# Optimization experiments

Measured on AMD Instinct MI355X. Metric: run time of the kernel, lower is better.

## Reference

```python
import jax, jax.numpy as jnp
import numpy as np
from jax import lax

B, C, H, W = 4, 512, 32, 32
HEADS, HC, GROUPS = 8, 64, 4
GC = C // GROUPS          # group channels = 128
GH = HEADS // GROUPS      # heads per group = 2
KK = 5                    # offset conv kernel (stage_idx=2)
OFFSET_RANGE_FACTOR = 2.0
LN_EPS = 1e-5


def conv1x1(x, w, b):
    # x: [B,Cin,H,W], w: [Cout,Cin], b: [Cout]
    return jnp.einsum('bchw,oc->bohw', x, w) + b[None, :, None, None]


def ref_points(h, w, n, dtype=jnp.float32):
    # torch linspace(0.5, h-0.5, h) normalized to (-1,1); stacked (y,x)
    ry = ((jnp.arange(h, dtype=dtype) + 0.5) / h) * 2.0 - 1.0
    rx = ((jnp.arange(w, dtype=dtype) + 0.5) / w) * 2.0 - 1.0
    ref = jnp.stack(jnp.meshgrid(ry, rx, indexing='ij'), axis=-1)  # [h,w,2]
    return jnp.broadcast_to(ref[None], (n, h, w, 2))


def grid_sample(img, grid):
    # F.grid_sample: bilinear, align_corners=True, padding_mode='zeros'
    # img: [N,C,Hs,Ws], grid: [N,*S,2] with grid[...,0]=x, grid[...,1]=y in [-1,1]
    N, Cc, Hs, Ws = img.shape
    gx = (grid[..., 0] + 1.0) * 0.5 * (Ws - 1)
    gy = (grid[..., 1] + 1.0) * 0.5 * (Hs - 1)
    x0 = jnp.floor(gx)
    y0 = jnp.floor(gy)
    wx1 = gx - x0
    wy1 = gy - y0
    imgf = img.reshape(N, Cc, Hs * Ws)

    def corner(ix, iy, wgt):
        valid = ((ix >= 0) & (ix <= Ws - 1) & (iy >= 0) & (iy <= Hs - 1)).astype(img.dtype)
        flat = (jnp.clip(iy, 0, Hs - 1) * Ws + jnp.clip(ix, 0, Ws - 1)).astype(jnp.int32)
        vals = jax.vmap(lambda im, f: im[:, f])(imgf, flat)  # [N,C,*S]
        return vals * (wgt * valid)[:, None]

    return (corner(x0, y0, (1 - wx1) * (1 - wy1))
            + corner(x0 + 1, y0, wx1 * (1 - wy1))
            + corner(x0, y0 + 1, (1 - wx1) * wy1)
            + corner(x0 + 1, y0 + 1, wx1 * wy1))


def setup_inputs() -> dict:
    key = jax.random.key(0)
    ks = jax.random.split(key, 10)

    def w(k, shape, s=0.02):
        return jax.random.normal(k, shape, jnp.float32) * s

    return {
        'x': jax.random.normal(ks[0], (B, C, H, W), jnp.float32),
        'w_q': w(ks[1], (C, C)), 'b_q': jnp.zeros((C,), jnp.float32),
        'w_k': w(ks[2], (C, C)), 'b_k': jnp.zeros((C,), jnp.float32),
        'w_v': w(ks[3], (C, C)), 'b_v': jnp.zeros((C,), jnp.float32),
        'w_o': w(ks[4], (C, C)), 'b_o': jnp.zeros((C,), jnp.float32),
        'dw_w': w(ks[5], (GC, 1, KK, KK), 0.05),  # depthwise offset conv
        'dw_b': jnp.zeros((GC,), jnp.float32),
        'ln_g': jnp.ones((GC,), jnp.float32),
        'ln_b': jnp.zeros((GC,), jnp.float32),
        'off_w': w(ks[6], (2, GC), 0.05),          # 1x1 conv -> 2 offset channels
        'rpe': w(ks[7], (HEADS, 2 * H - 1, 2 * W - 1), 0.01),
    }


def reference(x, w_q, b_q, w_k, b_k, w_v, b_v, w_o, b_o,
              dw_w, dw_b, ln_g, ln_b, off_w, rpe):
    q = conv1x1(x, w_q, b_q)
    # 'b (g c) h w -> (b g) c h w'
    q_off = q.reshape(B * GROUPS, GC, H, W)
    # depthwise conv kk=5, stride=1, pad=2
    off = lax.conv_general_dilated(q_off, dw_w, (1, 1),
                                   ((KK // 2, KK // 2), (KK // 2, KK // 2)),
                                   dimension_numbers=('NCHW', 'OIHW', 'NCHW'),
                                   feature_group_count=GC) + dw_b[None, :, None, None]
    # LayerNormProxy over channel dim
    mu = jnp.mean(off, axis=1, keepdims=True)
    var = jnp.mean((off - mu) ** 2, axis=1, keepdims=True)
    off = (off - mu) * lax.rsqrt(var + LN_EPS) * ln_g[None, :, None, None] + ln_b[None, :, None, None]
    off = jax.nn.gelu(off, approximate=False)
    off = jnp.einsum('bchw,oc->bohw', off, off_w)  # [B*G, 2, Hk, Wk] (y,x channels)
    Hk, Wk = off.shape[2], off.shape[3]
    nS = Hk * Wk
    off_range = jnp.array([1.0 / Hk, 1.0 / Wk], dtype=x.dtype).reshape(1, 2, 1, 1)
    off = jnp.tanh(off) * off_range * OFFSET_RANGE_FACTOR
    off = jnp.transpose(off, (0, 2, 3, 1))  # [B*G, Hk, Wk, 2]
    ref = ref_points(Hk, Wk, B * GROUPS, x.dtype)
    pos = off + ref  # offset_range_factor >= 0 branch
    # deformable sampling (grid takes (x,y))
    xs = grid_sample(x.reshape(B * GROUPS, GC, H, W), pos[..., ::-1])  # [B*G,GC,Hk,Wk]
    xs = xs.reshape(B, C, 1, nS)
    qf = q.reshape(B * HEADS, HC, H * W)
    k = conv1x1(xs, w_k, b_k).reshape(B * HEADS, HC, nS)
    v = conv1x1(xs, w_v, b_v).reshape(B * HEADS, HC, nS)
    attn = jnp.einsum('bcm,bcn->bmn', qf, k) * (HC ** -0.5)  # [B*Hd, HW, nS]
    # continuous relative-position bias via bilinear table lookup
    rpe_b = jnp.broadcast_to(rpe[None], (B,) + rpe.shape).reshape(
        B * GROUPS, GH, rpe.shape[1], rpe.shape[2])
    q_grid = ref_points(H, W, B * GROUPS, x.dtype)
    disp = (q_grid.reshape(B * GROUPS, H * W, 1, 2)
            - pos.reshape(B * GROUPS, 1, nS, 2)) * 0.5  # [B*G, HW, nS, 2]
    bias = grid_sample(rpe_b, disp[..., ::-1]).reshape(B * HEADS, H * W, nS)
    attn = jax.nn.softmax(attn + bias, axis=2)
    out = jnp.einsum('bmn,bcn->bcm', attn, v).reshape(B, C, H, W)
    y = conv1x1(out, w_o, b_o)
    return (y,
            pos.reshape(B, GROUPS, Hk, Wk, 2),
            ref.reshape(B, GROUPS, Hk, Wk, 2))
```

## Files before the change

### kernel.cpp

```cpp
#include <hip/hip_runtime.h>
#include <hip/hip_bf16.h>

typedef __hip_bfloat16 bf16;
typedef __attribute__((ext_vector_type(8))) short bf16x8;
typedef __attribute__((ext_vector_type(4))) float f32x4;

#define BDIM 4
#define CDIM 512
#define NHEADS 8
#define NGROUPS 4
#define GCH 128

__device__ __forceinline__ float bf2f(bf16 v) { return __bfloat162float(v); }
__device__ __forceinline__ float bfu2f(unsigned short u) {
  return __uint_as_float(((unsigned)u) << 16);
}
__device__ __forceinline__ unsigned short f2bu(float v) {
  return __hip_bfloat16_raw(__float2bfloat16(v)).x;
}
__device__ __forceinline__ unsigned pack2(float lo, float hi) {
  return (unsigned)f2bu(lo) | ((unsigned)f2bu(hi) << 16);
}

template <bool IN_F32, typename OutT, int NMAT>
__global__ __launch_bounds__(256) void gemm_kernel(
    const float* __restrict__ W0, const float* __restrict__ bias0,
    const float* __restrict__ W1, const float* __restrict__ bias1,
    const void* __restrict__ in,
    OutT* __restrict__ out0, OutT* __restrict__ out1) {
  __shared__ __align__(16) unsigned char smem[8192 * (NMAT + 1)];
  unsigned char* b_lds = smem + 8192 * NMAT;
  const int b = blockIdx.z;
  const int o0 = blockIdx.y * 64;
  const int n0 = blockIdx.x * 64;
  const int t = threadIdx.x, l = t & 63, w = t >> 6;
  const int rg = l >> 4, cl = l & 15;
  const int o_base = (w >> 1) * 32, n_base = (w & 1) * 32;
  const int ao = t >> 2;
  const int ac8 = (t & 3) * 8;
  const int kc2 = (t & 31) * 2;
  const int kn8 = (t >> 5) * 8;
  const unsigned swo = (unsigned)((ao & 7) << 4);
  const float* Ws[2] = {W0, W1};
  const float* Bs[2] = {bias0, bias1};
  OutT* Os[2] = {out0, out1};

  f32x4 acc[NMAT][2][2];
#pragma unroll
  for (int m = 0; m < NMAT; m++)
#pragma unroll
    for (int i = 0; i < 2; i++)
#pragma unroll
      for (int j = 0; j < 2; j++) acc[m][i][j] = {0.f, 0.f, 0.f, 0.f};

  for (int k0 = 0; k0 < 512; k0 += 64) {
#pragma unroll
    for (int m = 0; m < NMAT; m++) {
      const float* wr = Ws[m] + (size_t)(o0 + ao) * 512 + k0;
      const float4 a0 = *(const float4*)(wr + ac8);
      const float4 a1 = *(const float4*)(wr + ac8 + 4);
      const float4 c0 = *(const float4*)(wr + ac8 + 32);
      const float4 c1 = *(const float4*)(wr + ac8 + 36);
      uint4 ua = {pack2(a0.x, a0.y), pack2(a0.z, a0.w),
                  pack2(a1.x, a1.y), pack2(a1.z, a1.w)};
      uint4 ub = {pack2(c0.x, c0.y), pack2(c0.z, c0.w),
                  pack2(c1.x, c1.y), pack2(c1.z, c1.w)};
      unsigned char* am = smem + 8192 * m;
      *(uint4*)(am + ao * 128 + ((2 * ac8) ^ swo)) = ua;
      *(uint4*)(am + ao * 128 + ((2 * ac8 + 64) ^ swo)) = ub;
    }
    if constexpr (IN_F32) {
      const float* inb = (const float*)in + (size_t)b * 524288;
      const float* p0 = inb + (size_t)(k0 + kc2) * 1024 + n0 + kn8;
      union { float4 v[2]; float f[8]; } r0, r1;
      r0.v[0] = *(const float4*)p0;
      r0.v[1] = *(const float4*)(p0 + 4);
      r1.v[0] = *(const float4*)(p0 + 1024);
      r1.v[1] = *(const float4*)(p0 + 1028);
#pragma unroll
      for (int i = 0; i < 8; i++) {
        const int n = kn8 + i;
        *(unsigned*)(b_lds + n * 128 + ((2 * kc2) ^ ((n & 7) << 4))) =
            pack2(r0.f[i], r1.f[i]);
      }
    } else {
      const unsigned short* inb = (const unsigned short*)in + (size_t)b * 524288;
      union { uint4 v; unsigned short hw[8]; } r0, r1;
      r0.v = *(const uint4*)(inb + (size_t)(k0 + kc2) * 1024 + n0 + kn8);
      r1.v = *(const uint4*)(inb + (size_t)(k0 + kc2 + 1) * 1024 + n0 + kn8);
#pragma unroll
      for (int i = 0; i < 8; i++) {
        const int n = kn8 + i;
        const unsigned v32 = (unsigned)r0.hw[i] | ((unsigned)r1.hw[i] << 16);
        *(unsigned*)(b_lds + n * 128 + ((2 * kc2) ^ ((n & 7) << 4))) = v32;
      }
    }
    __syncthreads();
#pragma unroll
    for (int kk = 0; kk < 2; kk++) {
      bf16x8 bfr[2];
#pragma unroll
      for (int nn = 0; nn < 2; nn++) {
        const int n_loc = n_base + 16 * nn + cl;
        bfr[nn] = *(const bf16x8*)(b_lds + n_loc * 128 +
                                   ((64 * kk + 16 * rg) ^ ((n_loc & 7) << 4)));
      }
#pragma unroll
      for (int m = 0; m < NMAT; m++) {
        bf16x8 af[2];
#pragma unroll
        for (int mi = 0; mi < 2; mi++) {
          const int o_loc = o_base + 16 * mi + cl;
          af[mi] = *(const bf16x8*)(smem + 8192 * m + o_loc * 128 +
                                    ((64 * kk + 16 * rg) ^ ((o_loc & 7) << 4)));
        }
#pragma unroll
        for (int mi = 0; mi < 2; mi++)
#pragma unroll
          for (int nn = 0; nn < 2; nn++)
            acc[m][mi][nn] = __builtin_amdgcn_mfma_f32_16x16x32_bf16(
                af[mi], bfr[nn], acc[m][mi][nn], 0, 0, 0);
      }
    }
    __syncthreads();
  }

  float* o_st = (float*)smem;
#pragma unroll
  for (int m = 0; m < NMAT; m++) {
    __syncthreads();
#pragma unroll
    for (int mi = 0; mi < 2; mi++)
#pragma unroll
      for (int nn = 0; nn < 2; nn++)
#pragma unroll
        for (int r = 0; r < 4; r++)
          o_st[(o_base + 16 * mi + 4 * rg + r) * 64 + n_base + 16 * nn + cl] =
              acc[m][mi][nn][r];
    __syncthreads();
    const int eo = t >> 4;
    const int en = (t & 15) * 4;
#pragma unroll
    for (int pass = 0; pass < 4; pass++) {
      const int o_loc = eo + pass * 16;
      const f32x4 v = *(const f32x4*)(o_st + o_loc * 64 + en);
      const float bv = Bs[m][o0 + o_loc];
      if constexpr (sizeof(OutT) == 2) {
        ushort4 u;
        u.x = f2bu(v[0] + bv);
        u.y = f2bu(v[1] + bv);
        u.z = f2bu(v[2] + bv);
        u.w = f2bu(v[3] + bv);
        *(ushort4*)((bf16*)Os[m] + ((size_t)b * 512 + o0 + o_loc) * 1024 + n0 + en) = u;
      } else {
        float4 r = {v[0] + bv, v[1] + bv, v[2] + bv, v[3] + bv};
        *(float4*)((float*)Os[m] + ((size_t)b * 512 + o0 + o_loc) * 1024 + n0 + en) = r;
      }
    }
  }
}

__global__ __launch_bounds__(1024) void offset_kernel(
    const bf16* __restrict__ q, const float* __restrict__ dw_w,
    const float* __restrict__ dw_b, const float* __restrict__ ln_g,
    const float* __restrict__ ln_b, const float* __restrict__ off_w,
    float* __restrict__ pos, float* __restrict__ out_pos, float* __restrict__ out_ref) {
  __shared__ unsigned short q_s[5][36][128];
  __shared__ float red_a[8][2][2];
  __shared__ float red_p[8][2][2];
  const int bg = blockIdx.x;
  const int h = blockIdx.y;
  const int b = bg >> 2, g = bg & 3;
  const int t = threadIdx.x;

  for (int task = t; task < 640; task += 1024) {
    const int ky = task >> 7, c = task & 127;
    const int y = h + ky - 2;
    if (y >= 0 && y < 32) {
      const unsigned short* qrow =
          (const unsigned short*)q + ((size_t)b * CDIM + g * GCH + c) * 1024 + y * 32;
      q_s[ky][0][c] = 0;
      q_s[ky][1][c] = 0;
#pragma unroll
      for (int x8 = 0; x8 < 4; x8++) {
        union { uint4 u; unsigned short s[8]; } vv;
        vv.u = *(const uint4*)(qrow + x8 * 8);
#pragma unroll
        for (int i = 0; i < 8; i++) q_s[ky][2 + x8 * 8 + i][c] = vv.s[i];
      }
      q_s[ky][34][c] = 0;
      q_s[ky][35][c] = 0;
    } else {
#pragma unroll
      for (int xi = 0; xi < 36; xi++) q_s[ky][xi][c] = 0;
    }
  }

  const int wslot = t >> 7;
  const int c = t & 127;
  const int half = c >> 6;
  const int lane = t & 63;
  float wgt[25];
#pragma unroll
  for (int i = 0; i < 25; i++) wgt[i] = dw_w[c * 25 + i];
  const float cbias = dw_b[c];
  const float gam = ln_g[c], bet = ln_b[c];
  const float ow0 = off_w[c], ow1 = off_w[GCH + c];
  __syncthreads();

  for (int j = 0; j < 4; j++) {
    const int w = wslot * 4 + j;
    float s = cbias;
#pragma unroll
    for (int ky = 0; ky < 5; ky++)
#pragma unroll
      for (int kx = 0; kx < 5; kx++)
        s += wgt[ky * 5 + kx] * bfu2f(q_s[ky][w + kx][c]);
    float ssum = s, ssq = s * s;
#pragma unroll
    for (int o = 1; o < 64; o <<= 1) {
      ssum += __shfl_xor(ssum, o);
      ssq += __shfl_xor(ssq, o);
    }
    if (lane == 0) { red_a[wslot][half][0] = ssum; red_a[wslot][half][1] = ssq; }
    __syncthreads();
    const float mu = (red_a[wslot][0][0] + red_a[wslot][1][0]) * (1.0f / 128.0f);
    const float var = (red_a[wslot][0][1] + red_a[wslot][1][1]) * (1.0f / 128.0f) - mu * mu;
    const float xn = (s - mu) * rsqrtf(var + 1e-5f) * gam + bet;
    const float ge = 0.5f * xn * (1.0f + erff(xn * 0.70710678118654752f));
    float p0 = ow0 * ge, p1 = ow1 * ge;
#pragma unroll
    for (int o = 1; o < 64; o <<= 1) {
      p0 += __shfl_xor(p0, o);
      p1 += __shfl_xor(p1, o);
    }
    if (lane == 0) { red_p[wslot][half][0] = p0; red_p[wslot][half][1] = p1; }
    __syncthreads();
    if (c == 0) {
      const float oy = tanhf(red_p[wslot][0][0] + red_p[wslot][1][0]) * 0.0625f;
      const float ox = tanhf(red_p[wslot][0][1] + red_p[wslot][1][1]) * 0.0625f;
      const float ry = ((float)h + 0.5f) * (2.0f / 32.0f) - 1.0f;
      const float rx = ((float)w + 0.5f) * (2.0f / 32.0f) - 1.0f;
      const float py = oy + ry, px = ox + rx;
      const size_t idx = (size_t)bg * 1024 + h * 32 + w;
      pos[idx * 2] = py;
      pos[idx * 2 + 1] = px;
      out_pos[idx * 2] = py;
      out_pos[idx * 2 + 1] = px;
      out_ref[idx * 2] = ry;
      out_ref[idx * 2 + 1] = rx;
    }
  }
}

__global__ __launch_bounds__(256) void sample_kernel(
    const float* __restrict__ x, const float* __restrict__ pos, bf16* __restrict__ xs) {
  const int bg = blockIdx.x, c = blockIdx.y;
  const int b = bg >> 2, g = bg & 3;
  __shared__ float plane[1024];
  const float* xp = x + ((size_t)b * CDIM + g * GCH + c) * 1024;
  for (int i = threadIdx.x; i < 1024; i += 256) plane[i] = xp[i];
  __syncthreads();
  for (int s = threadIdx.x; s < 1024; s += 256) {
    const float py = pos[((size_t)bg * 1024 + s) * 2];
    const float px = pos[((size_t)bg * 1024 + s) * 2 + 1];
    const float gx = (px + 1.0f) * 15.5f;
    const float gy = (py + 1.0f) * 15.5f;
    const float x0f = floorf(gx), y0f = floorf(gy);
    const float wx = gx - x0f, wy = gy - y0f;
    const int ix = (int)x0f, iy = (int)y0f;
    float r = 0.0f;
    const bool vx0 = (ix >= 0) & (ix <= 31), vx1 = (ix + 1 >= 0) & (ix + 1 <= 31);
    const bool vy0 = (iy >= 0) & (iy <= 31), vy1 = (iy + 1 >= 0) & (iy + 1 <= 31);
    if (vy0 && vx0) r += plane[iy * 32 + ix] * (1.0f - wx) * (1.0f - wy);
    if (vy0 && vx1) r += plane[iy * 32 + ix + 1] * wx * (1.0f - wy);
    if (vy1 && vx0) r += plane[(iy + 1) * 32 + ix] * (1.0f - wx) * wy;
    if (vy1 && vx1) r += plane[(iy + 1) * 32 + ix + 1] * wx * wy;
    xs[((size_t)bg * GCH + c) * 1024 + s] = __float2bfloat16(r);
  }
}

__global__ __launch_bounds__(512) void attn_kernel(
    const bf16* __restrict__ q, const bf16* __restrict__ kk,
    const bf16* __restrict__ vv, const float* __restrict__ pos,
    const float* __restrict__ rpe, bf16* __restrict__ ao) {
  __shared__ __align__(16) unsigned char smem[68360];
  float* rpe_f = (float*)(smem + 49152);
  float* m_x = (float*)(smem + 67336);
  float* s_x = (float*)(smem + 67848);

  const int bh = blockIdx.y;
  const int m0 = blockIdx.x * 64;
  const int b = bh >> 3, h = bh & 7;
  const int g = h >> 1;
  const int bg = b * 4 + g;
  const int t = threadIdx.x, l = t & 63, w = t >> 6;
  const int wq = w & 3, half = w >> 2;
  const int rg = l >> 4, cl = l & 15;
  const int t2 = t & 255;
  const size_t hbase = ((size_t)b * CDIM + h * 64) * 1024;
  const unsigned short* qu = (const unsigned short*)q;

  unsigned char* k_base = smem + half * 8192;
  unsigned char* v_base = smem + 16384 + half * 8192;
  unsigned char* p_base = smem + 32768 + half * 8192;
  float* pos_a = (float*)(smem + 66312) + half * 128;

  for (int i = t; i < 65 * 66; i += 512) {
    const int y = i / 66, x = i - y * 66;
    float v = 0.0f;
    if (y >= 1 && y <= 63 && x >= 1 && x <= 63)
      v = rpe[h * 3969 + (y - 1) * 63 + (x - 1)];
    rpe_f[i] = v;
  }

  const int qloc = 16 * wq + cl;
  const int qm = m0 + qloc;
  const float qy15 = 15.5f * (((float)(qm >> 5) + 0.5f) * (2.0f / 32.0f) - 1.0f);
  const float qx15 = 15.5f * (((float)(qm & 31) + 0.5f) * (2.0f / 32.0f) - 1.0f);

  bf16x8 bq[2];
#pragma unroll
  for (int kc = 0; kc < 2; kc++) {
    bf16x8 a;
#pragma unroll
    for (int j = 0; j < 8; j++)
      a[j] = (short)qu[hbase + (size_t)(32 * kc + 8 * rg + j) * 1024 + qm];
    bq[kc] = a;
  }

  float rmax = -1e30f, rsum = 0.0f;
  f32x4 oacc[4] = {{0.f,0.f,0.f,0.f},{0.f,0.f,0.f,0.f},
                   {0.f,0.f,0.f,0.f},{0.f,0.f,0.f,0.f}};

  const float* posb = pos + (size_t)bg * 2048;
  const unsigned swl = (unsigned)((cl & 7) << 4);
  const int kc2 = (t2 & 31) * 2;
  const int kn8 = (t2 >> 5) * 8;
  const int vc = t2 >> 2;
  const int vh = (t2 & 3) * 32;

  for (int tile = 0; tile < 8; tile++) {
    const int n0 = half * 512 + tile * 64;
    {
      union { uint4 v; unsigned short hw[8]; } r0, r1;
      r0.v = *(const uint4*)(kk + hbase + (size_t)kc2 * 1024 + n0 + kn8);
      r1.v = *(const uint4*)(kk + hbase + (size_t)(kc2 + 1) * 1024 + n0 + kn8);
#pragma unroll
      for (int i = 0; i < 8; i++) {
        const int n = kn8 + i;
        const unsigned v32 = (unsigned)r0.hw[i] | ((unsigned)r1.hw[i] << 16);
        *(unsigned*)(k_base + n * 128 + ((kc2 * 2) ^ ((n & 7) << 4))) = v32;
      }
      const uint4 s0 = *(const uint4*)(vv + hbase + (size_t)vc * 1024 + n0 + vh / 2);
      const uint4 s1 = *(const uint4*)(vv + hbase + (size_t)vc * 1024 + n0 + vh / 2 + 8);
      *(uint4*)(v_base + vc * 128 + (vh ^ ((vc & 7) << 4))) = s0;
      *(uint4*)(v_base + vc * 128 + ((vh + 16) ^ ((vc & 7) << 4))) = s1;
      if (t2 < 128) pos_a[t2] = 31.0f - 15.5f * posb[2 * n0 + t2];
    }
    __syncthreads();

    f32x4 sf[4];
#pragma unroll
    for (int tn = 0; tn < 4; tn++) {
      const int nrow = 16 * tn + cl;
      const bf16x8 a0 = *(const bf16x8*)(k_base + nrow * 128 + ((16 * rg) ^ swl));
      const bf16x8 a1 = *(const bf16x8*)(k_base + nrow * 128 + ((64 + 16 * rg) ^ swl));
      f32x4 z = {0.f, 0.f, 0.f, 0.f};
      z = __builtin_amdgcn_mfma_f32_16x16x32_bf16(a0, bq[0], z, 0, 0, 0);
      z = __builtin_amdgcn_mfma_f32_16x16x32_bf16(a1, bq[1], z, 0, 0, 0);
      sf[tn] = z;
    }

#pragma unroll
    for (int tn = 0; tn < 4; tn++)
#pragma unroll
      for (int r = 0; r < 4; r++) {
        const int key = 16 * tn + 4 * rg + r;
        const float gyc = qy15 + pos_a[2 * key];
        const float gxc = qx15 + pos_a[2 * key + 1];
        const float y0f = floorf(gyc), x0f = floorf(gxc);
        const float wy = gyc - y0f, wx = gxc - x0f;
        const int iy1 = (int)y0f + 1, ix1 = (int)x0f + 1;
        const float* tp = rpe_f + iy1 * 66 + ix1;
        const float t00 = tp[0], t01 = tp[1];
        const float t10 = tp[66], t11 = tp[67];
        const float r0v = t00 + (t01 - t00) * wx;
        const float r1v = t10 + (t11 - t10) * wx;
        const float bias = r0v + (r1v - r0v) * wy;
        sf[tn][r] = sf[tn][r] * 0.125f + bias;
      }

    float tmax = sf[0][0];
#pragma unroll
    for (int tn = 0; tn < 4; tn++)
#pragma unroll
      for (int r = 0; r < 4; r++) tmax = fmaxf(tmax, sf[tn][r]);
    tmax = fmaxf(tmax, __shfl_xor(tmax, 16));
    tmax = fmaxf(tmax, __shfl_xor(tmax, 32));
    const float nmax = fmaxf(rmax, tmax);
    const float corr = __expf(rmax - nmax);
    rmax = nmax;
    float lsum = 0.0f;
    unsigned pw[8];
#pragma unroll
    for (int tn = 0; tn < 4; tn++) {
      const float p0 = __expf(sf[tn][0] - nmax);
      const float p1 = __expf(sf[tn][1] - nmax);
      const float p2 = __expf(sf[tn][2] - nmax);
      const float p3 = __expf(sf[tn][3] - nmax);
      lsum += (p0 + p1) + (p2 + p3);
      pw[2 * tn] = pack2(p0, p1);
      pw[2 * tn + 1] = pack2(p2, p3);
    }
    lsum += __shfl_xor(lsum, 16);
    lsum += __shfl_xor(lsum, 32);
    rsum = rsum * corr + lsum;
#pragma unroll
    for (int tc = 0; tc < 4; tc++) {
      oacc[tc][0] *= corr; oacc[tc][1] *= corr;
      oacc[tc][2] *= corr; oacc[tc][3] *= corr;
    }

#pragma unroll
    for (int tn = 0; tn < 4; tn++) {
      *(unsigned*)(p_base + qloc * 128 + ((2 * (16 * tn + 4 * rg)) ^ swl)) = pw[2 * tn];
      *(unsigned*)(p_base + qloc * 128 + ((2 * (16 * tn + 4 * rg) + 4) ^ swl)) = pw[2 * tn + 1];
    }

#pragma unroll
    for (int kc = 0; kc < 2; kc++) {
      const bf16x8 pb = *(const bf16x8*)(p_base + qloc * 128 + ((2 * (32 * kc + 8 * rg)) ^ swl));
#pragma unroll
      for (int tc = 0; tc < 4; tc++) {
        const int crow = 16 * tc + cl;
        const bf16x8 av = *(const bf16x8*)(v_base + crow * 128 + ((2 * (32 * kc + 8 * rg)) ^ swl));
        oacc[tc] = __builtin_amdgcn_mfma_f32_16x16x32_bf16(av, pb, oacc[tc], 0, 0, 0);
      }
    }
    __syncthreads();
  }

  if (l < 16) {
    m_x[half * 64 + wq * 16 + cl] = rmax;
    s_x[half * 64 + wq * 16 + cl] = rsum;
  }
  __syncthreads();
  const float m0v = m_x[wq * 16 + cl], m1v = m_x[64 + wq * 16 + cl];
  const float s0v = s_x[wq * 16 + cl], s1v = s_x[64 + wq * 16 + cl];
  const float M = fmaxf(m0v, m1v);
  const float f0 = __expf(m0v - M), f1 = __expf(m1v - M);
  const float inv = 1.0f / (f0 * s0v + f1 * s1v);
  const float scale = (half == 0 ? f0 : f1) * inv;
  float* o_st = (float*)smem;
  if (half == 0) {
#pragma unroll
    for (int tc = 0; tc < 4; tc++)
#pragma unroll
      for (int r = 0; r < 4; r++)
        o_st[(16 * tc + 4 * rg + r) * 66 + qloc] = oacc[tc][r] * scale;
  }
  __syncthreads();
  if (half == 1) {
#pragma unroll
    for (int tc = 0; tc < 4; tc++)
#pragma unroll
      for (int r = 0; r < 4; r++)
        o_st[(16 * tc + 4 * rg + r) * 66 + qloc] += oacc[tc][r] * scale;
  }
  __syncthreads();
  {
    const int c = t >> 3, mq = (t & 7) * 8;
    unsigned u[4];
#pragma unroll
    for (int i = 0; i < 4; i++)
      u[i] = pack2(o_st[c * 66 + mq + 2 * i], o_st[c * 66 + mq + 2 * i + 1]);
    uint4 outv = {u[0], u[1], u[2], u[3]};
    *(uint4*)(ao + hbase + (size_t)c * 1024 + m0 + mq) = outv;
  }
}

extern "C" void kernel_launch(void* const* d_in, const int* in_sizes, int n_in,
                              void* d_out, int out_size, void* d_ws, size_t ws_size,
                              hipStream_t stream) {
  const float* x    = (const float*)d_in[0];
  const float* w_q  = (const float*)d_in[1];
  const float* b_q  = (const float*)d_in[2];
  const float* w_k  = (const float*)d_in[3];
  const float* b_k  = (const float*)d_in[4];
  const float* w_v  = (const float*)d_in[5];
  const float* b_v  = (const float*)d_in[6];
  const float* w_o  = (const float*)d_in[7];
  const float* b_o  = (const float*)d_in[8];
  const float* dw_w = (const float*)d_in[9];
  const float* dw_b = (const float*)d_in[10];
  const float* ln_g = (const float*)d_in[11];
  const float* ln_b = (const float*)d_in[12];
  const float* off_w= (const float*)d_in[13];
  const float* rpe  = (const float*)d_in[14];

  float* out_y   = (float*)d_out;
  float* out_pos = out_y + 2097152;
  float* out_ref = out_pos + 32768;

  float* pos_ws = (float*)d_ws;
  bf16*  q_ws   = (bf16*)(pos_ws + 32768);
  bf16*  xs_ws  = q_ws + 2097152;
  bf16*  k_ws   = xs_ws + 2097152;
  bf16*  v_ws   = k_ws + 2097152;
  bf16*  ao_ws  = xs_ws;

  gemm_kernel<true, bf16, 1><<<dim3(16, 8, 4), 256, 0, stream>>>(
      w_q, b_q, nullptr, nullptr, x, q_ws, (bf16*)nullptr);
  offset_kernel<<<dim3(16, 32), 1024, 0, stream>>>(q_ws, dw_w, dw_b, ln_g, ln_b, off_w,
                                                   pos_ws, out_pos, out_ref);
  sample_kernel<<<dim3(16, 128), 256, 0, stream>>>(x, pos_ws, xs_ws);
  gemm_kernel<false, bf16, 2><<<dim3(16, 8, 4), 256, 0, stream>>>(
      w_k, b_k, w_v, b_v, xs_ws, k_ws, v_ws);
  attn_kernel<<<dim3(16, 32), 512, 0, stream>>>(q_ws, k_ws, v_ws, pos_ws, rpe, ao_ws);
  gemm_kernel<false, float, 1><<<dim3(16, 8, 4), 256, 0, stream>>>(
      w_o, b_o, nullptr, nullptr, ao_ws, out_y, (float*)nullptr);
}
```

Measured before the change: 111.8 us.

## Split GEMM K dimension across two thread halves with LDS reduction

Measured after the change: 114.3 us. +2.3%, slower.

```diff
diff --git a/kernel.cpp b/kernel.cpp
--- a/kernel.cpp
+++ b/kernel.cpp
@@ -23,27 +23,30 @@
 }
 
 template <bool IN_F32, typename OutT, int NMAT>
-__global__ __launch_bounds__(256) void gemm_kernel(
+__global__ __launch_bounds__(512) void gemm_kernel(
     const float* __restrict__ W0, const float* __restrict__ bias0,
     const float* __restrict__ W1, const float* __restrict__ bias1,
     const void* __restrict__ in,
     OutT* __restrict__ out0, OutT* __restrict__ out1) {
-  __shared__ __align__(16) unsigned char smem[8192 * (NMAT + 1)];
-  unsigned char* b_lds = smem + 8192 * NMAT;
+  __shared__ __align__(16) unsigned char smem[16384 * (NMAT + 1)];
   const int b = blockIdx.z;
   const int o0 = blockIdx.y * 64;
   const int n0 = blockIdx.x * 64;
   const int t = threadIdx.x, l = t & 63, w = t >> 6;
+  const int ks = t >> 8;
+  const int t2 = t & 255;
+  const int quad = w & 3;
   const int rg = l >> 4, cl = l & 15;
-  const int o_base = (w >> 1) * 32, n_base = (w & 1) * 32;
-  const int ao = t >> 2;
-  const int ac8 = (t & 3) * 8;
-  const int kc2 = (t & 31) * 2;
-  const int kn8 = (t >> 5) * 8;
+  const int o_base = (quad >> 1) * 32, n_base = (quad & 1) * 32;
+  const int ao = t2 >> 2;
+  const int ac8 = (t2 & 3) * 8;
+  const int kc2 = (t2 & 31) * 2;
+  const int kn8 = (t2 >> 5) * 8;
   const unsigned swo = (unsigned)((ao & 7) << 4);
   const float* Ws[2] = {W0, W1};
   const float* Bs[2] = {bias0, bias1};
   OutT* Os[2] = {out0, out1};
+  unsigned char* bl = smem + NMAT * 16384 + ks * 8192;
 
   f32x4 acc[NMAT][2][2];
 #pragma unroll
@@ -53,7 +56,8 @@
 #pragma unroll
       for (int j = 0; j < 2; j++) acc[m][i][j] = {0.f, 0.f, 0.f, 0.f};
 
-  for (int k0 = 0; k0 < 512; k0 += 64) {
+  for (int it = 0; it < 4; it++) {
+    const int k0 = ks * 256 + it * 64;
 #pragma unroll
     for (int m = 0; m < NMAT; m++) {
       const float* wr = Ws[m] + (size_t)(o0 + ao) * 512 + k0;
@@ -65,7 +69,7 @@
                   pack2(a1.x, a1.y), pack2(a1.z, a1.w)};
       uint4 ub = {pack2(c0.x, c0.y), pack2(c0.z, c0.w),
                   pack2(c1.x, c1.y), pack2(c1.z, c1.w)};
-      unsigned char* am = smem + 8192 * m;
+      unsigned char* am = smem + (m * 2 + ks) * 8192;
       *(uint4*)(am + ao * 128 + ((2 * ac8) ^ swo)) = ua;
       *(uint4*)(am + ao * 128 + ((2 * ac8 + 64) ^ swo)) = ub;
     }
@@ -80,7 +84,7 @@
 #pragma unroll
       for (int i = 0; i < 8; i++) {
         const int n = kn8 + i;
-        *(unsigned*)(b_lds + n * 128 + ((2 * kc2) ^ ((n & 7) << 4))) =
+        *(unsigned*)(bl + n * 128 + ((2 * kc2) ^ ((n & 7) << 4))) =
             pack2(r0.f[i], r1.f[i]);
       }
     } else {
@@ -92,7 +96,7 @@
       for (int i = 0; i < 8; i++) {
         const int n = kn8 + i;
         const unsigned v32 = (unsigned)r0.hw[i] | ((unsigned)r1.hw[i] << 16);
-        *(unsigned*)(b_lds + n * 128 + ((2 * kc2) ^ ((n & 7) << 4))) = v32;
+        *(unsigned*)(bl + n * 128 + ((2 * kc2) ^ ((n & 7) << 4))) = v32;
       }
     }
     __syncthreads();
@@ -102,7 +106,7 @@
 #pragma unroll
       for (int nn = 0; nn < 2; nn++) {
         const int n_loc = n_base + 16 * nn + cl;
-        bfr[nn] = *(const bf16x8*)(b_lds + n_loc * 128 +
+        bfr[nn] = *(const bf16x8*)(bl + n_loc * 128 +
                                    ((64 * kk + 16 * rg) ^ ((n_loc & 7) << 4)));
       }
 #pragma unroll
@@ -111,7 +115,7 @@
 #pragma unroll
         for (int mi = 0; mi < 2; mi++) {
           const int o_loc = o_base + 16 * mi + cl;
-          af[mi] = *(const bf16x8*)(smem + 8192 * m + o_loc * 128 +
+          af[mi] = *(const bf16x8*)(smem + (m * 2 + ks) * 8192 + o_loc * 128 +
                                     ((64 * kk + 16 * rg) ^ ((o_loc & 7) << 4)));
         }
 #pragma unroll
@@ -128,33 +132,45 @@
   float* o_st = (float*)smem;
 #pragma unroll
   for (int m = 0; m < NMAT; m++) {
-    __syncthreads();
-#pragma unroll
-    for (int mi = 0; mi < 2; mi++)
-#pragma unroll
-      for (int nn = 0; nn < 2; nn++)
-#pragma unroll
-        for (int r = 0; r < 4; r++)
-          o_st[(o_base + 16 * mi + 4 * rg + r) * 64 + n_base + 16 * nn + cl] =
-              acc[m][mi][nn][r];
-    __syncthreads();
-    const int eo = t >> 4;
-    const int en = (t & 15) * 4;
-#pragma unroll
-    for (int pass = 0; pass < 4; pass++) {
-      const int o_loc = eo + pass * 16;
-      const f32x4 v = *(const f32x4*)(o_st + o_loc * 64 + en);
+    if (m) __syncthreads();
+    if (ks == 0) {
+#pragma unroll
+      for (int mi = 0; mi < 2; mi++)
+#pragma unroll
+        for (int nn = 0; nn < 2; nn++)
+#pragma unroll
+          for (int r = 0; r < 4; r++)
+            o_st[(o_base + 16 * mi + 4 * rg + r) * 64 + n_base + 16 * nn + cl] =
+                acc[m][mi][nn][r];
+    }
+    __syncthreads();
+    if (ks == 1) {
+#pragma unroll
+      for (int mi = 0; mi < 2; mi++)
+#pragma unroll
+        for (int nn = 0; nn < 2; nn++)
+#pragma unroll
+          for (int r = 0; r < 4; r++)
+            o_st[(o_base + 16 * mi + 4 * rg + r) * 64 + n_base + 16 * nn + cl] +=
+                acc[m][mi][nn][r];
+    }
+    __syncthreads();
+    {
+      const int o_loc = t >> 3;
+      const int en = (t & 7) * 8;
+      const f32x4 v0 = *(const f32x4*)(o_st + o_loc * 64 + en);
+      const f32x4 v1 = *(const f32x4*)(o_st + o_loc * 64 + en + 4);
       const float bv = Bs[m][o0 + o_loc];
       if constexpr (sizeof(OutT) == 2) {
-        ushort4 u;
-        u.x = f2bu(v[0] + bv);
-        u.y = f2bu(v[1] + bv);
-        u.z = f2bu(v[2] + bv);
-        u.w = f2bu(v[3] + bv);
-        *(ushort4*)((bf16*)Os[m] + ((size_t)b * 512 + o0 + o_loc) * 1024 + n0 + en) = u;
+        uint4 u = {pack2(v0[0] + bv, v0[1] + bv), pack2(v0[2] + bv, v0[3] + bv),
+                   pack2(v1[0] + bv, v1[1] + bv), pack2(v1[2] + bv, v1[3] + bv)};
+        *(uint4*)((bf16*)Os[m] + ((size_t)b * 512 + o0 + o_loc) * 1024 + n0 + en) = u;
       } else {
-        float4 r = {v[0] + bv, v[1] + bv, v[2] + bv, v[3] + bv};
-        *(float4*)((float*)Os[m] + ((size_t)b * 512 + o0 + o_loc) * 1024 + n0 + en) = r;
+        float4 r0 = {v0[0] + bv, v0[1] + bv, v0[2] + bv, v0[3] + bv};
+        float4 r1 = {v1[0] + bv, v1[1] + bv, v1[2] + bv, v1[3] + bv};
+        float* dst = (float*)Os[m] + ((size_t)b * 512 + o0 + o_loc) * 1024 + n0 + en;
+        *(float4*)dst = r0;
+        *(float4*)(dst + 4) = r1;
       }
     }
   }
@@ -510,14 +526,14 @@
   bf16*  v_ws   = k_ws + 2097152;
   bf16*  ao_ws  = xs_ws;
 
-  gemm_kernel<true, bf16, 1><<<dim3(16, 8, 4), 256, 0, stream>>>(
+  gemm_kernel<true, bf16, 1><<<dim3(16, 8, 4), 512, 0, stream>>>(
       w_q, b_q, nullptr, nullptr, x, q_ws, (bf16*)nullptr);
   offset_kernel<<<dim3(16, 32), 1024, 0, stream>>>(q_ws, dw_w, dw_b, ln_g, ln_b, off_w,
                                                    pos_ws, out_pos, out_ref);
   sample_kernel<<<dim3(16, 128), 256, 0, stream>>>(x, pos_ws, xs_ws);
-  gemm_kernel<false, bf16, 2><<<dim3(16, 8, 4), 256, 0, stream>>>(
+  gemm_kernel<false, bf16, 2><<<dim3(16, 8, 4), 512, 0, stream>>>(
       w_k, b_k, w_v, b_v, xs_ws, k_ws, v_ws);
   attn_kernel<<<dim3(16, 32), 512, 0, stream>>>(q_ws, k_ws, v_ws, pos_ws, rpe, ao_ws);
-  gemm_kernel<false, float, 1><<<dim3(16, 8, 4), 256, 0, stream>>>(
+  gemm_kernel<false, float, 1><<<dim3(16, 8, 4), 512, 0, stream>>>(
       w_o, b_o, nullptr, nullptr, ao_ws, out_y, (float*)nullptr);
 }
```
